# Performance work log

Hardware: AMD Instinct MI355X
Metric: run time of the kernel (lower is better)

Reference implementation:

```python
import jax, jax.numpy as jnp
import numpy as np

B, S, D = 8, 2048, 128

def setup_inputs() -> dict:
    key = jax.random.key(0)
    kq, kk, kv = jax.random.split(key, 3)
    return {
        "Q": jax.random.normal(kq, (B, S, D), dtype=jnp.float32),
        "K": jax.random.normal(kk, (B, S, D), dtype=jnp.float32),
        "V": jax.random.normal(kv, (B, S, D), dtype=jnp.float32),
    }

def reference(Q, K, V):
    dim = Q.shape[-1]
    scores = jnp.einsum('bqd,bkd->bqk', Q, K) / jnp.sqrt(jnp.float32(dim))
    seq_len = Q.shape[1]
    # causal mask: -inf above the diagonal (matches torch.triu(ones*-inf, diagonal=1))
    causal = jnp.triu(jnp.full((seq_len, seq_len), -jnp.inf, dtype=scores.dtype), k=1)
    scores = scores + causal
    weights = jax.nn.softmax(scores, axis=-1)
    context = jnp.einsum('bqk,bkd->bqd', weights, V)
    return context
```

## Files before the change

### kernel.cpp

```cpp
#include <hip/hip_runtime.h>

#define B_ 8
#define S_ 2048
#define D_ 128
#define NT_ 64
#define FRAG_ 512

typedef __attribute__((ext_vector_type(4))) float f32x4;
typedef __attribute__((ext_vector_type(16))) float f32x16;
typedef __attribute__((ext_vector_type(8))) short bf16x8;
typedef __attribute__((ext_vector_type(2))) unsigned uint32x2;

__device__ __forceinline__ short f2bf(float f) {
  union { float f; unsigned u; } x; x.f = f;
  unsigned r = x.u + 0x7FFFu + ((x.u >> 16) & 1u);
  return (short)(r >> 16);
}

__device__ __forceinline__ unsigned cvt_pk_bf16(float lo, float hi) {
  unsigned r;
  asm("v_cvt_pk_bf16_f32 %0, %1, %2" : "=v"(r) : "v"(lo), "v"(hi));
  return r;
}

__device__ __forceinline__ void plswap(unsigned& a, unsigned& b, int hi) {
#if __has_builtin(__builtin_amdgcn_permlane32_swap)
  uint32x2 r = __builtin_amdgcn_permlane32_swap(a, b, false, false);
  a = r[0]; b = r[1];
#else
  unsigned pa = (unsigned)__shfl_xor((int)a, 32, 64);
  unsigned pb = (unsigned)__shfl_xor((int)b, 32, 64);
  unsigned na = hi ? pb : a;
  unsigned nb = hi ? b : pa;
  a = na; b = nb;
#endif
}

__device__ __forceinline__ f32x16 zero16() {
  f32x16 v = {0.f,0.f,0.f,0.f,0.f,0.f,0.f,0.f,0.f,0.f,0.f,0.f,0.f,0.f,0.f,0.f};
  return v;
}

__global__ __launch_bounds__(256) void prep_frag(
    const float* __restrict__ Q, const float* __restrict__ K,
    const float* __restrict__ V, short* __restrict__ Qf,
    short* __restrict__ Kf, short* __restrict__ Vf) {
  __shared__ short qt[32][136], kt[32][136], vt[32][136];
  const int b  = blockIdx.x >> 6;
  const int st = blockIdx.x & 63;
  const int t  = threadIdx.x;
  const int row = t >> 3, c0 = (t & 7) * 16;
  const size_t base = ((size_t)(b * S_ + st * 32 + row)) * D_ + c0;
  const float scq = 0.12751744553939605f;

  #pragma unroll
  for (int i = 0; i < 4; ++i) {
    f32x4 q = *(const f32x4*)(Q + base + i * 4);
    f32x4 k = *(const f32x4*)(K + base + i * 4);
    f32x4 v = *(const f32x4*)(V + base + i * 4);
    #pragma unroll
    for (int j = 0; j < 4; ++j) {
      qt[row][c0 + i * 4 + j] = f2bf(q[j] * scq);
      kt[row][c0 + i * 4 + j] = f2bf(k[j]);
      vt[row][c0 + i * 4 + j] = f2bf(v[j]);
    }
  }
  __syncthreads();

  const int l = t & 63, ln = l & 31, hi = l >> 5, w = t >> 6;
  const size_t gidx = (size_t)(b * NT_ + st) * 8;
  #pragma unroll
  for (int i = 0; i < 2; ++i) {
    const int m = w * 2 + i;
    bf16x8 qv = *(const bf16x8*)&qt[ln][m * 16 + hi * 8];
    bf16x8 kv = *(const bf16x8*)&kt[ln][m * 16 + hi * 8];
    *(bf16x8*)(Qf + (gidx + m) * FRAG_ + l * 8) = qv;
    *(bf16x8*)(Kf + (gidx + m) * FRAG_ + l * 8) = kv;
    const int d4 = m >> 1, h = m & 1;
    bf16x8 vv;
    #pragma unroll
    for (int j = 0; j < 8; ++j) vv[j] = vt[h * 16 + hi * 8 + j][d4 * 32 + ln];
    *(bf16x8*)(Vf + (gidx + m) * FRAG_ + l * 8) = vv;
  }
}

__global__ __launch_bounds__(256, 2) void fattn_fwd(
    const short* __restrict__ Qf, const short* __restrict__ Kf,
    const short* __restrict__ Vf, float* __restrict__ Og) {
  const int task = blockIdx.x;
  const int j    = task >> 3;
  const int b    = task & 7;
  const int tt   = (j < 32) ? (2 * j) : (127 - 2 * j);
  const int q0   = tt * 32;
  const int tid  = threadIdx.x;
  const int w    = tid >> 6;
  const int lane = tid & 63;
  const int ln   = lane & 31;
  const int hi   = lane >> 5;

  const short* Qfb = Qf + (size_t)b * (NT_ * 8 * FRAG_);
  const short* Kfb = Kf + (size_t)b * (NT_ * 8 * FRAG_);
  const short* Vfb = Vf + (size_t)b * (NT_ * 8 * FRAG_);
  float*       Ob  = Og + (size_t)b * S_ * D_;

  __shared__ float ldsO[4][4][32][33];
  __shared__ float lS[4][32], invLS[32];

  bf16x8 qb[8];
  {
    const short* qfp = Qfb + (size_t)tt * (8 * FRAG_) + lane * 8;
    #pragma unroll
    for (int dt = 0; dt < 8; ++dt) qb[dt] = *(const bf16x8*)(qfp + dt * FRAG_);
  }

  f32x16 o[4];
  #pragma unroll
  for (int i = 0; i < 4; ++i) o[i] = zero16();
  float l_part = 0.f;

  int s = w;
  if (s <= tt) {
    const short* kfp = Kfb + (size_t)s * (8 * FRAG_) + lane * 8;
    bf16x8 kb[8];
    #pragma unroll
    for (int dt = 0; dt < 8; ++dt) kb[dt] = *(const bf16x8*)(kfp + dt * FRAG_);

    for (;;) {
      const short* vfp = Vfb + (size_t)s * (8 * FRAG_) + lane * 8;
      bf16x8 va[8];
      #pragma unroll
      for (int m8 = 0; m8 < 8; ++m8) va[m8] = *(const bf16x8*)(vfp + m8 * FRAG_);

      f32x16 accA = zero16(), accB = zero16();
      __builtin_amdgcn_s_setprio(1);
      #pragma unroll
      for (int dt = 0; dt < 8; dt += 2) {
        accA = __builtin_amdgcn_mfma_f32_32x32x16_bf16(kb[dt],     qb[dt],     accA, 0, 0, 0);
        accB = __builtin_amdgcn_mfma_f32_32x32x16_bf16(kb[dt + 1], qb[dt + 1], accB, 0, 0, 0);
      }
      __builtin_amdgcn_s_setprio(0);

      const bool last = (s + 4 > tt);
      if (!last) {
        const short* k2 = Kfb + (size_t)(s + 4) * (8 * FRAG_) + lane * 8;
        #pragma unroll
        for (int dt = 0; dt < 8; ++dt) kb[dt] = *(const bf16x8*)(k2 + dt * FRAG_);
      }

      f32x16 sv = accA + accB;

      if (s == tt) {
        #pragma unroll
        for (int r = 0; r < 16; ++r) {
          const int kl = (r & 3) + 8 * (r >> 2) + 4 * hi;
          if (kl > ln) sv[r] = -512.0f;
        }
      }

      float p[16];
      #pragma unroll
      for (int r = 0; r < 16; ++r) p[r] = exp2f(sv[r]);
      float ts[8];
      #pragma unroll
      for (int r = 0; r < 8; ++r) ts[r] = p[r] + p[r + 8];
      #pragma unroll
      for (int r = 0; r < 4; ++r) ts[r] = ts[r] + ts[r + 4];
      l_part += (ts[0] + ts[1]) + (ts[2] + ts[3]);

      unsigned x0 = cvt_pk_bf16(p[0], p[1]);
      unsigned x1 = cvt_pk_bf16(p[2], p[3]);
      unsigned y0 = cvt_pk_bf16(p[4], p[5]);
      unsigned y1 = cvt_pk_bf16(p[6], p[7]);
      plswap(x0, y0, hi);
      plswap(x1, y1, hi);
      unsigned z0 = cvt_pk_bf16(p[8], p[9]);
      unsigned z1 = cvt_pk_bf16(p[10], p[11]);
      unsigned w0 = cvt_pk_bf16(p[12], p[13]);
      unsigned w1 = cvt_pk_bf16(p[14], p[15]);
      plswap(z0, w0, hi);
      plswap(z1, w1, hi);
      union { unsigned u[4]; bf16x8 v; } pb0, pb1;
      pb0.u[0] = x0; pb0.u[1] = x1; pb0.u[2] = y0; pb0.u[3] = y1;
      pb1.u[0] = z0; pb1.u[1] = z1; pb1.u[2] = w0; pb1.u[3] = w1;

      __builtin_amdgcn_s_setprio(1);
      #pragma unroll
      for (int d4 = 0; d4 < 4; ++d4) {
        o[d4] = __builtin_amdgcn_mfma_f32_32x32x16_bf16(va[d4 * 2],     pb0.v, o[d4], 0, 0, 0);
        o[d4] = __builtin_amdgcn_mfma_f32_32x32x16_bf16(va[d4 * 2 + 1], pb1.v, o[d4], 0, 0, 0);
      }
      __builtin_amdgcn_s_setprio(0);

      if (last) break;
      s += 4;
    }
  }

  float l = l_part + __shfl_xor(l_part, 32, 64);
  if (hi == 0) lS[w][ln] = l;
  #pragma unroll
  for (int d4 = 0; d4 < 4; ++d4)
    #pragma unroll
    for (int r = 0; r < 16; ++r)
      ldsO[w][d4][ln][(r & 3) + 8 * (r >> 2) + 4 * hi] = o[d4][r];
  __syncthreads();

  if (tid < 32) {
    const float L = lS[0][tid] + lS[1][tid] + lS[2][tid] + lS[3][tid];
    invLS[tid] = 1.0f / L;
  }
  __syncthreads();

  #pragma unroll
  for (int k = 0; k < 16; ++k) {
    const int e = k * 256 + tid;
    const int row = e >> 7;
    const int col = e & 127;
    float acc = 0.f;
    #pragma unroll
    for (int w2 = 0; w2 < 4; ++w2)
      acc += ldsO[w2][col >> 5][row][col & 31];
    Ob[(size_t)(q0 + row) * D_ + col] = acc * invLS[row];
  }
}

extern "C" void kernel_launch(void* const* d_in, const int* in_sizes, int n_in,
                              void* d_out, int out_size, void* d_ws, size_t ws_size,
                              hipStream_t stream) {
  const float* Q = (const float*)d_in[0];
  const float* K = (const float*)d_in[1];
  const float* V = (const float*)d_in[2];
  float* O = (float*)d_out;

  short* Qf = (short*)d_ws;
  short* Kf = Qf + (size_t)B_ * S_ * D_;
  short* Vf = Kf + (size_t)B_ * S_ * D_;

  prep_frag<<<B_ * NT_, 256, 0, stream>>>(Q, K, V, Qf, Kf, Vf);
  fattn_fwd<<<B_ * NT_, 256, 0, stream>>>(Qf, Kf, Vf, O);
}
```

Measured before the change: 30.50 us.

## Software-pipeline QK^T of next tile with PV of previous tile; use hardware exp

Restructures the per-wave key loop so the QK^T MFMAs for tile s+4 are interleaved with the PV MFMAs for tile s, with a prologue computing the first scores and an epilogue doing the final PV. The interleaving gives the matrix unit independent work while the softmax/exp/convert of each tile is hidden behind the other chain. It also replaces exp2f with a raw v_exp_f32, dropping the range-handling wrapper. The cost is more live registers (kb, va, pb and o at once), which could hurt occupancy at the two-blocks-per-CU launch bound.

```diff
diff --git a/kernel.cpp b/kernel.cpp
--- a/kernel.cpp
+++ b/kernel.cpp
@@ -11,10 +11,18 @@
 typedef __attribute__((ext_vector_type(8))) short bf16x8;
 typedef __attribute__((ext_vector_type(2))) unsigned uint32x2;
 
+#define MF(a, b, c) __builtin_amdgcn_mfma_f32_32x32x16_bf16(a, b, c, 0, 0, 0)
+
 __device__ __forceinline__ short f2bf(float f) {
   union { float f; unsigned u; } x; x.f = f;
   unsigned r = x.u + 0x7FFFu + ((x.u >> 16) & 1u);
   return (short)(r >> 16);
+}
+
+__device__ __forceinline__ float exp2_hw(float x) {
+  float r;
+  asm("v_exp_f32 %0, %1" : "=v"(r) : "v"(x));
+  return r;
 }
 
 __device__ __forceinline__ unsigned cvt_pk_bf16(float lo, float hi) {
@@ -118,48 +126,41 @@
   for (int i = 0; i < 4; ++i) o[i] = zero16();
   float l_part = 0.f;
 
-  int s = w;
-  if (s <= tt) {
-    const short* kfp = Kfb + (size_t)s * (8 * FRAG_) + lane * 8;
-    bf16x8 kb[8];
-    #pragma unroll
-    for (int dt = 0; dt < 8; ++dt) kb[dt] = *(const bf16x8*)(kfp + dt * FRAG_);
-
-    for (;;) {
-      const short* vfp = Vfb + (size_t)s * (8 * FRAG_) + lane * 8;
-      bf16x8 va[8];
+  const int s0 = w;
+  if (s0 <= tt) {
+    bf16x8 kb[8], va[8];
+    union { unsigned u[4]; bf16x8 v; } pb0, pb1;
+
+    {
+      const short* kfp = Kfb + (size_t)s0 * (8 * FRAG_) + lane * 8;
+      #pragma unroll
+      for (int dt = 0; dt < 8; ++dt) kb[dt] = *(const bf16x8*)(kfp + dt * FRAG_);
+
+      f32x16 sv = zero16();
+      __builtin_amdgcn_s_setprio(1);
+      #pragma unroll
+      for (int dt = 0; dt < 8; ++dt) sv = MF(kb[dt], qb[dt], sv);
+      __builtin_amdgcn_s_setprio(0);
+
+      const short* vfp = Vfb + (size_t)s0 * (8 * FRAG_) + lane * 8;
       #pragma unroll
       for (int m8 = 0; m8 < 8; ++m8) va[m8] = *(const bf16x8*)(vfp + m8 * FRAG_);
-
-      f32x16 accA = zero16(), accB = zero16();
-      __builtin_amdgcn_s_setprio(1);
-      #pragma unroll
-      for (int dt = 0; dt < 8; dt += 2) {
-        accA = __builtin_amdgcn_mfma_f32_32x32x16_bf16(kb[dt],     qb[dt],     accA, 0, 0, 0);
-        accB = __builtin_amdgcn_mfma_f32_32x32x16_bf16(kb[dt + 1], qb[dt + 1], accB, 0, 0, 0);
-      }
-      __builtin_amdgcn_s_setprio(0);
-
-      const bool last = (s + 4 > tt);
-      if (!last) {
-        const short* k2 = Kfb + (size_t)(s + 4) * (8 * FRAG_) + lane * 8;
+      if (s0 + 4 <= tt) {
+        const short* k2 = Kfb + (size_t)(s0 + 4) * (8 * FRAG_) + lane * 8;
         #pragma unroll
         for (int dt = 0; dt < 8; ++dt) kb[dt] = *(const bf16x8*)(k2 + dt * FRAG_);
       }
 
-      f32x16 sv = accA + accB;
-
-      if (s == tt) {
+      if (s0 == tt) {
         #pragma unroll
         for (int r = 0; r < 16; ++r) {
           const int kl = (r & 3) + 8 * (r >> 2) + 4 * hi;
           if (kl > ln) sv[r] = -512.0f;
         }
       }
-
       float p[16];
       #pragma unroll
-      for (int r = 0; r < 16; ++r) p[r] = exp2f(sv[r]);
+      for (int r = 0; r < 16; ++r) p[r] = exp2_hw(sv[r]);
       float ts[8];
       #pragma unroll
       for (int r = 0; r < 8; ++r) ts[r] = p[r] + p[r + 8];
@@ -167,33 +168,72 @@
       for (int r = 0; r < 4; ++r) ts[r] = ts[r] + ts[r + 4];
       l_part += (ts[0] + ts[1]) + (ts[2] + ts[3]);
 
-      unsigned x0 = cvt_pk_bf16(p[0], p[1]);
-      unsigned x1 = cvt_pk_bf16(p[2], p[3]);
-      unsigned y0 = cvt_pk_bf16(p[4], p[5]);
-      unsigned y1 = cvt_pk_bf16(p[6], p[7]);
-      plswap(x0, y0, hi);
-      plswap(x1, y1, hi);
-      unsigned z0 = cvt_pk_bf16(p[8], p[9]);
-      unsigned z1 = cvt_pk_bf16(p[10], p[11]);
-      unsigned w0 = cvt_pk_bf16(p[12], p[13]);
-      unsigned w1 = cvt_pk_bf16(p[14], p[15]);
-      plswap(z0, w0, hi);
-      plswap(z1, w1, hi);
-      union { unsigned u[4]; bf16x8 v; } pb0, pb1;
+      unsigned x0 = cvt_pk_bf16(p[0], p[1]),  x1 = cvt_pk_bf16(p[2], p[3]);
+      unsigned y0 = cvt_pk_bf16(p[4], p[5]),  y1 = cvt_pk_bf16(p[6], p[7]);
+      plswap(x0, y0, hi); plswap(x1, y1, hi);
+      unsigned z0 = cvt_pk_bf16(p[8], p[9]),  z1 = cvt_pk_bf16(p[10], p[11]);
+      unsigned w0 = cvt_pk_bf16(p[12], p[13]), w1 = cvt_pk_bf16(p[14], p[15]);
+      plswap(z0, w0, hi); plswap(z1, w1, hi);
       pb0.u[0] = x0; pb0.u[1] = x1; pb0.u[2] = y0; pb0.u[3] = y1;
       pb1.u[0] = z0; pb1.u[1] = z1; pb1.u[2] = w0; pb1.u[3] = w1;
-
+    }
+
+    for (int v = s0 + 4; v <= tt; v += 4) {
+      f32x16 acc = zero16();
       __builtin_amdgcn_s_setprio(1);
-      #pragma unroll
-      for (int d4 = 0; d4 < 4; ++d4) {
-        o[d4] = __builtin_amdgcn_mfma_f32_32x32x16_bf16(va[d4 * 2],     pb0.v, o[d4], 0, 0, 0);
-        o[d4] = __builtin_amdgcn_mfma_f32_32x32x16_bf16(va[d4 * 2 + 1], pb1.v, o[d4], 0, 0, 0);
-      }
+      acc  = MF(kb[0], qb[0], acc);  o[0] = MF(va[0], pb0.v, o[0]);
+      acc  = MF(kb[1], qb[1], acc);  o[0] = MF(va[1], pb1.v, o[0]);
+      acc  = MF(kb[2], qb[2], acc);  o[1] = MF(va[2], pb0.v, o[1]);
+      acc  = MF(kb[3], qb[3], acc);  o[1] = MF(va[3], pb1.v, o[1]);
+      acc  = MF(kb[4], qb[4], acc);  o[2] = MF(va[4], pb0.v, o[2]);
+      acc  = MF(kb[5], qb[5], acc);  o[2] = MF(va[5], pb1.v, o[2]);
+      acc  = MF(kb[6], qb[6], acc);  o[3] = MF(va[6], pb0.v, o[3]);
+      acc  = MF(kb[7], qb[7], acc);  o[3] = MF(va[7], pb1.v, o[3]);
       __builtin_amdgcn_s_setprio(0);
 
-      if (last) break;
-      s += 4;
-    }
+      const short* vfp = Vfb + (size_t)v * (8 * FRAG_) + lane * 8;
+      #pragma unroll
+      for (int m8 = 0; m8 < 8; ++m8) va[m8] = *(const bf16x8*)(vfp + m8 * FRAG_);
+      if (v + 4 <= tt) {
+        const short* k2 = Kfb + (size_t)(v + 4) * (8 * FRAG_) + lane * 8;
+        #pragma unroll
+        for (int dt = 0; dt < 8; ++dt) kb[dt] = *(const bf16x8*)(k2 + dt * FRAG_);
+      }
+
+      if (v == tt) {
+        #pragma unroll
+        for (int r = 0; r < 16; ++r) {
+          const int kl = (r & 3) + 8 * (r >> 2) + 4 * hi;
+          if (kl > ln) acc[r] = -512.0f;
+        }
+      }
+      float p[16];
+      #pragma unroll
+      for (int r = 0; r < 16; ++r) p[r] = exp2_hw(acc[r]);
+      float ts[8];
+      #pragma unroll
+      for (int r = 0; r < 8; ++r) ts[r] = p[r] + p[r + 8];
+      #pragma unroll
+      for (int r = 0; r < 4; ++r) ts[r] = ts[r] + ts[r + 4];
+      l_part += (ts[0] + ts[1]) + (ts[2] + ts[3]);
+
+      unsigned x0 = cvt_pk_bf16(p[0], p[1]),  x1 = cvt_pk_bf16(p[2], p[3]);
+      unsigned y0 = cvt_pk_bf16(p[4], p[5]),  y1 = cvt_pk_bf16(p[6], p[7]);
+      plswap(x0, y0, hi); plswap(x1, y1, hi);
+      unsigned z0 = cvt_pk_bf16(p[8], p[9]),  z1 = cvt_pk_bf16(p[10], p[11]);
+      unsigned w0 = cvt_pk_bf16(p[12], p[13]), w1 = cvt_pk_bf16(p[14], p[15]);
+      plswap(z0, w0, hi); plswap(z1, w1, hi);
+      pb0.u[0] = x0; pb0.u[1] = x1; pb0.u[2] = y0; pb0.u[3] = y1;
+      pb1.u[0] = z0; pb1.u[1] = z1; pb1.u[2] = w0; pb1.u[3] = w1;
+    }
+
+    __builtin_amdgcn_s_setprio(1);
+    #pragma unroll
+    for (int d4 = 0; d4 < 4; ++d4) {
+      o[d4] = MF(va[d4 * 2],     pb0.v, o[d4]);
+      o[d4] = MF(va[d4 * 2 + 1], pb1.v, o[d4]);
+    }
+    __builtin_amdgcn_s_setprio(0);
   }
 
   float l = l_part + __shfl_xor(l_part, 32, 64);
```

Result: slower. 31.42 us (+3.0%).

## Pair complementary causal query tiles per block and use hardware exp2

Applied to the files above, without the earlier changes.

Each block now handles two query tiles, j and 63-j, in sequence, so every block does roughly equal causal work. The grid is halved to 256 blocks, giving one block per CU. The exp2f call is replaced with the raw v_exp_f32 instruction, and the launch-bounds occupancy hint is dropped. This trades fewer resident waves and less latency hiding for balanced per-block work and a cheaper exponential. It also adds a barrier between the two phases.

```diff
diff --git a/kernel.cpp b/kernel.cpp
--- a/kernel.cpp
+++ b/kernel.cpp
@@ -11,10 +11,18 @@
 typedef __attribute__((ext_vector_type(8))) short bf16x8;
 typedef __attribute__((ext_vector_type(2))) unsigned uint32x2;
 
+#define MF(a, b, c) __builtin_amdgcn_mfma_f32_32x32x16_bf16(a, b, c, 0, 0, 0)
+
 __device__ __forceinline__ short f2bf(float f) {
   union { float f; unsigned u; } x; x.f = f;
   unsigned r = x.u + 0x7FFFu + ((x.u >> 16) & 1u);
   return (short)(r >> 16);
+}
+
+__device__ __forceinline__ float exp2_hw(float x) {
+  float r;
+  asm("v_exp_f32 %0, %1" : "=v"(r) : "v"(x));
+  return r;
 }
 
 __device__ __forceinline__ unsigned cvt_pk_bf16(float lo, float hi) {
@@ -84,14 +92,12 @@
   }
 }
 
-__global__ __launch_bounds__(256, 2) void fattn_fwd(
+__global__ __launch_bounds__(256) void fattn_fwd(
     const short* __restrict__ Qf, const short* __restrict__ Kf,
     const short* __restrict__ Vf, float* __restrict__ Og) {
   const int task = blockIdx.x;
   const int j    = task >> 3;
   const int b    = task & 7;
-  const int tt   = (j < 32) ? (2 * j) : (127 - 2 * j);
-  const int q0   = tt * 32;
   const int tid  = threadIdx.x;
   const int w    = tid >> 6;
   const int lane = tid & 63;
@@ -106,121 +112,122 @@
   __shared__ float ldsO[4][4][32][33];
   __shared__ float lS[4][32], invLS[32];
 
-  bf16x8 qb[8];
-  {
-    const short* qfp = Qfb + (size_t)tt * (8 * FRAG_) + lane * 8;
-    #pragma unroll
-    for (int dt = 0; dt < 8; ++dt) qb[dt] = *(const bf16x8*)(qfp + dt * FRAG_);
-  }
-
-  f32x16 o[4];
-  #pragma unroll
-  for (int i = 0; i < 4; ++i) o[i] = zero16();
-  float l_part = 0.f;
-
-  int s = w;
-  if (s <= tt) {
-    const short* kfp = Kfb + (size_t)s * (8 * FRAG_) + lane * 8;
-    bf16x8 kb[8];
-    #pragma unroll
-    for (int dt = 0; dt < 8; ++dt) kb[dt] = *(const bf16x8*)(kfp + dt * FRAG_);
-
-    for (;;) {
-      const short* vfp = Vfb + (size_t)s * (8 * FRAG_) + lane * 8;
-      bf16x8 va[8];
-      #pragma unroll
-      for (int m8 = 0; m8 < 8; ++m8) va[m8] = *(const bf16x8*)(vfp + m8 * FRAG_);
-
-      f32x16 accA = zero16(), accB = zero16();
-      __builtin_amdgcn_s_setprio(1);
-      #pragma unroll
-      for (int dt = 0; dt < 8; dt += 2) {
-        accA = __builtin_amdgcn_mfma_f32_32x32x16_bf16(kb[dt],     qb[dt],     accA, 0, 0, 0);
-        accB = __builtin_amdgcn_mfma_f32_32x32x16_bf16(kb[dt + 1], qb[dt + 1], accB, 0, 0, 0);
+  #pragma unroll 1
+  for (int phase = 0; phase < 2; ++phase) {
+    const int tt = phase ? (63 - j) : j;
+    const int q0 = tt * 32;
+
+    bf16x8 qb[8];
+    {
+      const short* qfp = Qfb + (size_t)tt * (8 * FRAG_) + lane * 8;
+      #pragma unroll
+      for (int dt = 0; dt < 8; ++dt) qb[dt] = *(const bf16x8*)(qfp + dt * FRAG_);
+    }
+
+    f32x16 o[4];
+    #pragma unroll
+    for (int i = 0; i < 4; ++i) o[i] = zero16();
+    float l_part = 0.f;
+
+    int s = w;
+    if (s <= tt) {
+      const short* kfp = Kfb + (size_t)s * (8 * FRAG_) + lane * 8;
+      bf16x8 kb[8];
+      #pragma unroll
+      for (int dt = 0; dt < 8; ++dt) kb[dt] = *(const bf16x8*)(kfp + dt * FRAG_);
+
+      for (;;) {
+        const short* vfp = Vfb + (size_t)s * (8 * FRAG_) + lane * 8;
+        bf16x8 va[8];
+        #pragma unroll
+        for (int m8 = 0; m8 < 8; ++m8) va[m8] = *(const bf16x8*)(vfp + m8 * FRAG_);
+
+        f32x16 accA = zero16(), accB = zero16();
+        __builtin_amdgcn_s_setprio(1);
+        #pragma unroll
+        for (int dt = 0; dt < 8; dt += 2) {
+          accA = MF(kb[dt],     qb[dt],     accA);
+          accB = MF(kb[dt + 1], qb[dt + 1], accB);
+        }
+        __builtin_amdgcn_s_setprio(0);
+
+        const bool lastst = (s + 4 > tt);
+        if (!lastst) {
+          const short* k2 = Kfb + (size_t)(s + 4) * (8 * FRAG_) + lane * 8;
+          #pragma unroll
+          for (int dt = 0; dt < 8; ++dt) kb[dt] = *(const bf16x8*)(k2 + dt * FRAG_);
+        }
+
+        f32x16 sv = accA + accB;
+
+        if (s == tt) {
+          #pragma unroll
+          for (int r = 0; r < 16; ++r) {
+            const int kl = (r & 3) + 8 * (r >> 2) + 4 * hi;
+            if (kl > ln) sv[r] = -512.0f;
+          }
+        }
+
+        float p[16];
+        #pragma unroll
+        for (int r = 0; r < 16; ++r) p[r] = exp2_hw(sv[r]);
+        float ts[8];
+        #pragma unroll
+        for (int r = 0; r < 8; ++r) ts[r] = p[r] + p[r + 8];
+        #pragma unroll
+        for (int r = 0; r < 4; ++r) ts[r] = ts[r] + ts[r + 4];
+        l_part += (ts[0] + ts[1]) + (ts[2] + ts[3]);
+
+        unsigned x0 = cvt_pk_bf16(p[0], p[1]),  x1 = cvt_pk_bf16(p[2], p[3]);
+        unsigned y0 = cvt_pk_bf16(p[4], p[5]),  y1 = cvt_pk_bf16(p[6], p[7]);
+        plswap(x0, y0, hi); plswap(x1, y1, hi);
+        unsigned z0 = cvt_pk_bf16(p[8], p[9]),  z1 = cvt_pk_bf16(p[10], p[11]);
+        unsigned w0 = cvt_pk_bf16(p[12], p[13]), w1 = cvt_pk_bf16(p[14], p[15]);
+        plswap(z0, w0, hi); plswap(z1, w1, hi);
+        union { unsigned u[4]; bf16x8 v; } pb0, pb1;
+        pb0.u[0] = x0; pb0.u[1] = x1; pb0.u[2] = y0; pb0.u[3] = y1;
+        pb1.u[0] = z0; pb1.u[1] = z1; pb1.u[2] = w0; pb1.u[3] = w1;
+
+        __builtin_amdgcn_s_setprio(1);
+        #pragma unroll
+        for (int d4 = 0; d4 < 4; ++d4) {
+          o[d4] = MF(va[d4 * 2],     pb0.v, o[d4]);
+          o[d4] = MF(va[d4 * 2 + 1], pb1.v, o[d4]);
+        }
+        __builtin_amdgcn_s_setprio(0);
+
+        if (lastst) break;
+        s += 4;
       }
-      __builtin_amdgcn_s_setprio(0);
-
-      const bool last = (s + 4 > tt);
-      if (!last) {
-        const short* k2 = Kfb + (size_t)(s + 4) * (8 * FRAG_) + lane * 8;
-        #pragma unroll
-        for (int dt = 0; dt < 8; ++dt) kb[dt] = *(const bf16x8*)(k2 + dt * FRAG_);
-      }
-
-      f32x16 sv = accA + accB;
-
-      if (s == tt) {
-        #pragma unroll
-        for (int r = 0; r < 16; ++r) {
-          const int kl = (r & 3) + 8 * (r >> 2) + 4 * hi;
-          if (kl > ln) sv[r] = -512.0f;
-        }
-      }
-
-      float p[16];
-      #pragma unroll
-      for (int r = 0; r < 16; ++r) p[r] = exp2f(sv[r]);
-      float ts[8];
-      #pragma unroll
-      for (int r = 0; r < 8; ++r) ts[r] = p[r] + p[r + 8];
-      #pragma unroll
-      for (int r = 0; r < 4; ++r) ts[r] = ts[r] + ts[r + 4];
-      l_part += (ts[0] + ts[1]) + (ts[2] + ts[3]);
-
-      unsigned x0 = cvt_pk_bf16(p[0], p[1]);
-      unsigned x1 = cvt_pk_bf16(p[2], p[3]);
-      unsigned y0 = cvt_pk_bf16(p[4], p[5]);
-      unsigned y1 = cvt_pk_bf16(p[6], p[7]);
-      plswap(x0, y0, hi);
-      plswap(x1, y1, hi);
-      unsigned z0 = cvt_pk_bf16(p[8], p[9]);
-      unsigned z1 = cvt_pk_bf16(p[10], p[11]);
-      unsigned w0 = cvt_pk_bf16(p[12], p[13]);
-      unsigned w1 = cvt_pk_bf16(p[14], p[15]);
-      plswap(z0, w0, hi);
-      plswap(z1, w1, hi);
-      union { unsigned u[4]; bf16x8 v; } pb0, pb1;
-      pb0.u[0] = x0; pb0.u[1] = x1; pb0.u[2] = y0; pb0.u[3] = y1;
-      pb1.u[0] = z0; pb1.u[1] = z1; pb1.u[2] = w0; pb1.u[3] = w1;
-
-      __builtin_amdgcn_s_setprio(1);
-      #pragma unroll
-      for (int d4 = 0; d4 < 4; ++d4) {
-        o[d4] = __builtin_amdgcn_mfma_f32_32x32x16_bf16(va[d4 * 2],     pb0.v, o[d4], 0, 0, 0);
-        o[d4] = __builtin_amdgcn_mfma_f32_32x32x16_bf16(va[d4 * 2 + 1], pb1.v, o[d4], 0, 0, 0);
-      }
-      __builtin_amdgcn_s_setprio(0);
-
-      if (last) break;
-      s += 4;
-    }
-  }
-
-  float l = l_part + __shfl_xor(l_part, 32, 64);
-  if (hi == 0) lS[w][ln] = l;
-  #pragma unroll
-  for (int d4 = 0; d4 < 4; ++d4)
-    #pragma unroll
-    for (int r = 0; r < 16; ++r)
-      ldsO[w][d4][ln][(r & 3) + 8 * (r >> 2) + 4 * hi] = o[d4][r];
-  __syncthreads();
-
-  if (tid < 32) {
-    const float L = lS[0][tid] + lS[1][tid] + lS[2][tid] + lS[3][tid];
-    invLS[tid] = 1.0f / L;
-  }
-  __syncthreads();
-
-  #pragma unroll
-  for (int k = 0; k < 16; ++k) {
-    const int e = k * 256 + tid;
-    const int row = e >> 7;
-    const int col = e & 127;
-    float acc = 0.f;
-    #pragma unroll
-    for (int w2 = 0; w2 < 4; ++w2)
-      acc += ldsO[w2][col >> 5][row][col & 31];
-    Ob[(size_t)(q0 + row) * D_ + col] = acc * invLS[row];
+    }
+
+    float l = l_part + __shfl_xor(l_part, 32, 64);
+    if (hi == 0) lS[w][ln] = l;
+    #pragma unroll
+    for (int d4 = 0; d4 < 4; ++d4)
+      #pragma unroll
+      for (int r = 0; r < 16; ++r)
+        ldsO[w][d4][ln][(r & 3) + 8 * (r >> 2) + 4 * hi] = o[d4][r];
+    __syncthreads();
+
+    if (tid < 32) {
+      const float L = lS[0][tid] + lS[1][tid] + lS[2][tid] + lS[3][tid];
+      invLS[tid] = 1.0f / L;
+    }
+    __syncthreads();
+
+    #pragma unroll
+    for (int k = 0; k < 16; ++k) {
+      const int e = k * 256 + tid;
+      const int row = e >> 7;
+      const int col = e & 127;
+      float acc = 0.f;
+      #pragma unroll
+      for (int w2 = 0; w2 < 4; ++w2)
+        acc += ldsO[w2][col >> 5][row][col & 31];
+      Ob[(size_t)(q0 + row) * D_ + col] = acc * invLS[row];
+    }
+    __syncthreads();
   }
 }
 
@@ -237,5 +244,5 @@
   short* Vf = Kf + (size_t)B_ * S_ * D_;
 
   prep_frag<<<B_ * NT_, 256, 0, stream>>>(Q, K, V, Qf, Kf, Vf);
-  fattn_fwd<<<B_ * NT_, 256, 0, stream>>>(Qf, Kf, Vf, O);
-}
+  fattn_fwd<<<B_ * 32, 256, 0, stream>>>(Qf, Kf, Vf, O);
+}
```

Result: slower. 31.59 us (+3.6%).
